# Kernel optimization log

Hardware: AMD Instinct MI355X
Metric: run time of the kernel (lower is better)

Reference implementation:

```python
import jax, jax.numpy as jnp
import numpy as np
import math

B, T, C = 64, 1024, 12
D, H, L = 512, 8, 2
FFN = 4 * D
FC_HIDDEN, NUM_CLASSES = 256, 5
KERNEL = 25          # config.moving_average default
FACTOR = 3           # config.autocorrelation_factor default
TOP_K = int(FACTOR * math.log(T))
EPS = 1e-5
MIN_SCALE = 1e-10


def _sinusoidal_pos(n_pos, dim):
    # HF AutoformerSinusoidalPositionalEmbedding._init_weight (Marian-style: sin block then cos block)
    pos = np.arange(n_pos, dtype=np.float64)[:, None]
    j = np.arange(dim)[None, :]
    enc = pos / np.power(10000.0, 2 * (j // 2) / dim)
    half = dim // 2
    out = np.zeros((n_pos, dim), np.float32)
    out[:, :half] = np.sin(enc[:, 0::2])
    out[:, half:] = np.cos(enc[:, 1::2])
    return jnp.asarray(out)


def _layernorm(x, g, b):
    mu = jnp.mean(x, axis=-1, keepdims=True)
    var = jnp.mean(jnp.square(x - mu), axis=-1, keepdims=True)
    return (x - mu) * jax.lax.rsqrt(var + EPS) * g + b


def _series_decomp_seasonal(x):
    # moving-average trend with edge-replication padding; return seasonal = x - trend
    pad = (KERNEL - 1) // 2
    xp = jnp.pad(x, ((0, 0), (pad, pad), (0, 0)), mode='edge')
    cs = jnp.cumsum(xp, axis=1)
    cs = jnp.concatenate([jnp.zeros_like(cs[:, :1]), cs], axis=1)
    trend = (cs[:, KERNEL:] - cs[:, :-KERNEL]) / KERNEL
    return x - trend


def _autocorr_attention(h, w, b):
    # w: (4, D, D) q/k/v/out, b: (4, D). Eval-mode HF AutoformerAttention (per-batch delays).
    hd = D // H
    def split(t):
        return t.reshape(B, T, H, hd).transpose(0, 2, 1, 3)  # (B,H,T,hd)
    q = split(h @ w[0] + b[0])
    k = split(h @ w[1] + b[1])
    v = split(h @ w[2] + b[2])
    # period-based dependency discovery via FFT cross-correlation along time
    qf = jnp.fft.rfft(q, n=T, axis=2)
    kf = jnp.fft.rfft(k, n=T, axis=2)
    corr = jnp.fft.irfft(qf * jnp.conj(kf), n=T, axis=2)  # (B,H,T,hd)
    mean_corr = corr.mean(axis=(1, 3))                    # (B,T)
    top_vals, top_idx = jax.lax.top_k(mean_corr, TOP_K)   # (B,K)
    wts = jax.nn.softmax(top_vals, axis=-1)               # (B,K)
    t_idx = jnp.arange(T)
    agg = jnp.zeros_like(v)
    for i in range(TOP_K):  # small fixed K, mirrors HF loop; circular roll by -delay
        idx = (t_idx[None, :] + top_idx[:, i][:, None]) % T      # (B,T)
        rolled = jnp.take_along_axis(v, idx[:, None, :, None], axis=2)
        agg = agg + rolled * wts[:, i][:, None, None, None]
    out = agg.transpose(0, 2, 1, 3).reshape(B, T, D)
    return out @ w[3] + b[3]


def _forward(x, emb_w, emb_ln_g, emb_ln_b, attn_w, attn_b, ln_g, ln_b,
             fc1_w, fc1_b, fc2_w, fc2_b, head_w1, head_b1, head_w2, head_b2):
    # AutoformerMeanScaler (observed mask is all-ones): scale = mean |x| over time, loc = 0
    scale = jnp.clip(jnp.mean(jnp.abs(x), axis=1, keepdims=True), MIN_SCALE)  # (B,1,C)
    inputs = x / scale
    # static features: log1p(|loc|)=0 and log(scale), broadcast over time; lags=[0] -> lagged == inputs
    static = jnp.concatenate([jnp.zeros_like(scale), jnp.log(scale)], axis=-1)  # (B,1,2C)
    feats = jnp.broadcast_to(static, (B, T, 2 * C))
    ti = jnp.concatenate([inputs, feats], axis=-1)  # (B,T,3C)

    h = ti @ emb_w + _sinusoidal_pos(T, D)[None]
    h = _layernorm(h, emb_ln_g, emb_ln_b)

    for l in range(L):
        res = h
        a = _autocorr_attention(h, attn_w[l], attn_b[l])
        h = _layernorm(res + a, ln_g[l, 0], ln_b[l, 0])
        h = _series_decomp_seasonal(h)
        res = h
        f = jax.nn.gelu(h @ fc1_w[l] + fc1_b[l], approximate=False)
        h = res + f @ fc2_w[l] + fc2_b[l]
        h = _layernorm(h, ln_g[l, 1], ln_b[l, 1])
        h = _series_decomp_seasonal(h)

    feat = h.mean(axis=1)  # (B,D)
    return jax.nn.relu(feat @ head_w1 + head_b1) @ head_w2 + head_b2  # (B,num_classes)


def setup_inputs() -> dict:
    key = jax.random.key(0)
    ks = jax.random.split(key, 8)
    s = 0.02
    rn = lambda k, shape: jax.random.normal(k, shape, jnp.float32) * s
    return {
        'x': jax.random.normal(ks[0], (B, T, C), jnp.float32),
        'emb_w': rn(ks[1], (3 * C, D)),
        'emb_ln_g': jnp.ones((D,), jnp.float32),
        'emb_ln_b': jnp.zeros((D,), jnp.float32),
        'attn_w': rn(ks[2], (L, 4, D, D)),
        'attn_b': jnp.zeros((L, 4, D), jnp.float32),
        'ln_g': jnp.ones((L, 2, D), jnp.float32),
        'ln_b': jnp.zeros((L, 2, D), jnp.float32),
        'fc1_w': rn(ks[3], (L, D, FFN)),
        'fc1_b': jnp.zeros((L, FFN), jnp.float32),
        'fc2_w': rn(ks[4], (L, FFN, D)),
        'fc2_b': jnp.zeros((L, D), jnp.float32),
        'head_w1': rn(ks[5], (D, FC_HIDDEN)),
        'head_b1': jnp.zeros((FC_HIDDEN,), jnp.float32),
        'head_w2': rn(ks[6], (FC_HIDDEN, NUM_CLASSES)),
        'head_b2': jnp.zeros((NUM_CLASSES,), jnp.float32),
    }


def reference(x, emb_w, emb_ln_g, emb_ln_b, attn_w, attn_b, ln_g, ln_b,
              fc1_w, fc1_b, fc2_w, fc2_b, head_w1, head_b1, head_w2, head_b2):
    return _forward(x, emb_w, emb_ln_g, emb_ln_b, attn_w, attn_b, ln_g, ln_b,
                    fc1_w, fc1_b, fc2_w, fc2_b, head_w1, head_b1, head_w2, head_b2)
```

## Files before the change

kernel.cpp:

```cpp
#include <hip/hip_runtime.h>
#include <math.h>

#define CB 64
#define CT 1024
#define CCH 12
#define CD 512
#define CL 2
#define CFFN 2048
#define CFCH 256
#define CNC 5
#define CTOPK 20
#define CEPS 1e-5f

typedef __attribute__((ext_vector_type(8))) short bfrag;
typedef __attribute__((ext_vector_type(4))) float ffrag;

__device__ inline ushort bf16r(float f) {
  unsigned u = __float_as_uint(f);
  unsigned r = (u + 0x7FFFu + ((u >> 16) & 1u)) >> 16;
  return (ushort)r;
}
__device__ inline float bf16f(ushort h) { return __uint_as_float(((unsigned)h) << 16); }

__device__ __forceinline__ void gld16(const ushort* g, ushort* l) {
  __builtin_amdgcn_global_load_lds((__attribute__((address_space(1))) void*)g,
                                   (__attribute__((address_space(3))) void*)l,
                                   16, 0, 0);
}

struct c32 { float x, y; };
__device__ inline c32 cadd(c32 a, c32 b) { return c32{a.x + b.x, a.y + b.y}; }
__device__ inline c32 csub(c32 a, c32 b) { return c32{a.x - b.x, a.y - b.y}; }
__device__ inline c32 cmul(c32 a, c32 b) {
  return c32{a.x * b.x - a.y * b.y, a.x * b.y + a.y * b.x};
}
__device__ inline c32 cmulj(c32 a, c32 b) {
  return c32{a.x * b.x + a.y * b.y, a.y * b.x - a.x * b.y};
}
__device__ inline c32 mineg_i(c32 a) { return c32{a.y, -a.x}; }
__device__ inline c32 mul_i(c32 a) { return c32{-a.y, a.x}; }

#define ZIDX(p) ((p) + ((p) >> 4))

__device__ inline int drev4(int t) {
  return ((t & 3) << 8) | (((t >> 2) & 3) << 6) | (((t >> 4) & 3) << 4) |
         (((t >> 6) & 3) << 2) | ((t >> 8) & 3);
}

template <int INV>
__device__ inline void fft_stage(c32* zz, const c32* twl, int tid, int s) {
  int L = 1 << (2 * s);
  int j = tid & (L - 1);
  int g = tid >> (2 * s);
  int p0 = (g << (2 * s + 2)) + j;
  int tb = j << (8 - 2 * s);
  c32 w1 = twl[ZIDX(tb)], w2 = twl[ZIDX(2 * tb)], w3 = twl[ZIDX(3 * tb)];
  c32 b0 = zz[ZIDX(p0)], b1 = zz[ZIDX(p0 + L)], b2 = zz[ZIDX(p0 + 2 * L)],
      b3 = zz[ZIDX(p0 + 3 * L)];
  if (INV) { b1 = cmulj(b1, w1); b2 = cmulj(b2, w2); b3 = cmulj(b3, w3); }
  else     { b1 = cmul(b1, w1);  b2 = cmul(b2, w2);  b3 = cmul(b3, w3); }
  c32 e0 = cadd(b0, b2), e1 = csub(b0, b2), e2 = cadd(b1, b3), e3 = csub(b1, b3);
  c32 e3r = INV ? mul_i(e3) : mineg_i(e3);
  zz[ZIDX(p0)] = cadd(e0, e2);
  zz[ZIDX(p0 + L)] = cadd(e1, e3r);
  zz[ZIDX(p0 + 2 * L)] = csub(e0, e2);
  zz[ZIDX(p0 + 3 * L)] = csub(e1, e3r);
}

__device__ inline void unp_acc(const c32* zf, int w, c32& acc) {
  int wc = (1024 - w) & 1023;
  c32 Z1 = zf[ZIDX(w)];
  c32 Z2r = zf[ZIDX(wc)];
  c32 Z2 = c32{Z2r.x, -Z2r.y};
  c32 Qf = c32{0.5f * (Z1.x + Z2.x), 0.5f * (Z1.y + Z2.y)};
  c32 M = c32{Z1.x - Z2.x, Z1.y - Z2.y};
  c32 Kf = c32{0.5f * M.y, -0.5f * M.x};
  acc.x += Qf.x * Kf.x + Qf.y * Kf.y;
  acc.y += Qf.y * Kf.x - Qf.x * Kf.y;
}

__global__ __launch_bounds__(256) void k_twid(c32* __restrict__ tw) {
  int j = blockIdx.x * 256 + threadIdx.x;
  double a = -2.0 * 3.14159265358979323846 * (double)j / 1024.0;
  tw[j] = c32{(float)cos(a), (float)sin(a)};
}

__global__ __launch_bounds__(256) void k_scale(const float* __restrict__ x,
                                               float* __restrict__ sc,
                                               float* __restrict__ lg) {
  int b = blockIdx.x, tid = threadIdx.x;
  float acc[CCH];
#pragma unroll
  for (int c = 0; c < CCH; ++c) acc[c] = 0.f;
  const float* xb = x + (size_t)b * CT * CCH;
  for (int t = tid; t < CT; t += 256) {
    const float* row = xb + t * CCH;
#pragma unroll
    for (int c = 0; c < CCH; ++c) acc[c] += fabsf(row[c]);
  }
  __shared__ float red[256][CCH];
#pragma unroll
  for (int c = 0; c < CCH; ++c) red[tid][c] = acc[c];
  __syncthreads();
  for (int off = 128; off > 0; off >>= 1) {
    if (tid < off) {
#pragma unroll
      for (int c = 0; c < CCH; ++c) red[tid][c] += red[tid + off][c];
    }
    __syncthreads();
  }
  if (tid < CCH) {
    float s = fmaxf(red[0][tid] * (1.0f / CT), 1e-10f);
    sc[b * CCH + tid] = s;
    lg[b * CCH + tid] = logf(s);
  }
}

__global__ __launch_bounds__(512) void k_postab(float* __restrict__ pos) {
  int t = blockIdx.x;
  int d = threadIdx.x;
  double v;
  if (d < 256) {
    double w = pow(10000.0, -((double)d) / 256.0);
    v = sin((double)t * w);
  } else {
    double w = pow(10000.0, -((double)(d - 256)) / 256.0);
    v = cos((double)t * w);
  }
  pos[(size_t)t * CD + d] = (float)v;
}

__global__ __launch_bounds__(128) void k_embed(const float* __restrict__ x,
                                               const float* __restrict__ sc,
                                               const float* __restrict__ lg,
                                               const float* __restrict__ W,
                                               const float* __restrict__ postab,
                                               const float* __restrict__ g,
                                               const float* __restrict__ beta,
                                               float* __restrict__ h,
                                               ushort* __restrict__ h2) {
  int row = blockIdx.x;
  int b = row >> 10, t = row & 1023;
  int tid = threadIdx.x;
  __shared__ float xs[CCH], ls[CCH];
  if (tid < CCH) {
    float s = sc[b * CCH + tid];
    xs[tid] = x[(size_t)row * CCH + tid] / s;
    ls[tid] = lg[b * CCH + tid];
  }
  __syncthreads();
  int d0 = tid * 4;
  float4 p = *(const float4*)(postab + (size_t)t * CD + d0);
  float v0 = p.x, v1 = p.y, v2 = p.z, v3 = p.w;
#pragma unroll
  for (int c = 0; c < CCH; ++c) {
    float xc = xs[c], lc = ls[c];
    float4 w0 = *(const float4*)(W + (size_t)c * CD + d0);
    float4 w1 = *(const float4*)(W + (size_t)(24 + c) * CD + d0);
    v0 += xc * w0.x + lc * w1.x;
    v1 += xc * w0.y + lc * w1.y;
    v2 += xc * w0.z + lc * w1.z;
    v3 += xc * w0.w + lc * w1.w;
  }
  float s1 = v0 + v1 + v2 + v3;
  float s2 = v0 * v0 + v1 * v1 + v2 * v2 + v3 * v3;
  for (int off = 32; off > 0; off >>= 1) {
    s1 += __shfl_down(s1, off);
    s2 += __shfl_down(s2, off);
  }
  __shared__ float ws1[2], ws2[2], mv[2];
  int wid = tid >> 6, lane = tid & 63;
  if (lane == 0) { ws1[wid] = s1; ws2[wid] = s2; }
  __syncthreads();
  if (tid == 0) {
    float S1 = ws1[0] + ws1[1], S2 = ws2[0] + ws2[1];
    float mu = S1 * (1.0f / CD);
    float var = S2 * (1.0f / CD) - mu * mu;
    mv[0] = mu;
    mv[1] = 1.0f / sqrtf(var + CEPS);
  }
  __syncthreads();
  float mu = mv[0], ri = mv[1];
  float4 gg = *(const float4*)(g + d0);
  float4 bb = *(const float4*)(beta + d0);
  float4 o;
  o.x = (v0 - mu) * ri * gg.x + bb.x;
  o.y = (v1 - mu) * ri * gg.y + bb.y;
  o.z = (v2 - mu) * ri * gg.z + bb.z;
  o.w = (v3 - mu) * ri * gg.w + bb.w;
  *(float4*)(h + (size_t)row * CD + d0) = o;
  ushort4 hv = {bf16r(o.x), bf16r(o.y), bf16r(o.z), bf16r(o.w)};
  *(ushort4*)(h2 + (size_t)row * CD + d0) = hv;
}

__global__ __launch_bounds__(256) void k_cvtw(const float* __restrict__ W,
                                              ushort* __restrict__ W2,
                                              int K, int N) {
  __shared__ float tile[32][33];
  int tx = threadIdx.x & 31, ty = threadIdx.x >> 5;
  int n0 = blockIdx.x * 32, k0 = blockIdx.y * 32;
#pragma unroll
  for (int r = 0; r < 4; ++r)
    tile[ty * 4 + r][tx] = W[(size_t)(k0 + ty * 4 + r) * N + n0 + tx];
  __syncthreads();
#pragma unroll
  for (int r = 0; r < 4; ++r) {
    int nl = ty * 4 + r, kl = tx;
    W2[(size_t)(n0 + nl) * K + k0 + kl] = bf16r(tile[kl][nl]);
  }
}

template <int EPI>
__global__ __launch_bounds__(256) void k_gemm3(const ushort* __restrict__ A,
                                               const ushort* __restrict__ W,
                                               const float* __restrict__ bias,
                                               const float* __restrict__ R,
                                               float* __restrict__ Cf,
                                               ushort* __restrict__ Cs,
                                               ushort* __restrict__ Cs2,
                                               int lda, int ldb, int ldc, int K) {
  __shared__ ushort AhS[2][128 * 32];
  __shared__ ushort BhS[2][128 * 32];
  int tid = threadIdx.x;
  int nx = gridDim.x;
  int nwg = nx * gridDim.y;
  int flat = blockIdx.y * nx + blockIdx.x;
  int sw = (flat & 7) * (nwg >> 3) + (flat >> 3);
  int n0 = (sw % nx) * 128, m0 = (sw / nx) * 128;
  int wid = __builtin_amdgcn_readfirstlane(tid >> 6);
  int lane = tid & 63;
  int lr = lane >> 2;
  int lc = ((lane & 3) ^ ((lr >> 2) & 3)) * 8;
  int wm = wid >> 1, wn = wid & 1;
  int mOff = wm * 64, nOff = wn * 64;
  int quad = lane >> 4, l16 = lane & 15;

  const ushort* pA = A + (size_t)(m0 + wid * 32 + lr) * lda + lc;
  const ushort* pB = W + (size_t)(n0 + wid * 32 + lr) * ldb + lc;
  const int NK = K >> 5;

  ffrag acc[4][4];
#pragma unroll
  for (int i = 0; i < 4; ++i)
#pragma unroll
    for (int j = 0; j < 4; ++j) acc[i][j] = (ffrag)(0.f);

#define ISSUE(t, buf)                                                        \
  {                                                                          \
    int kk = (t) << 5;                                                       \
    ushort* lA = &AhS[buf][(wid * 32) * 32];                                 \
    ushort* lB = &BhS[buf][(wid * 32) * 32];                                 \
    gld16(pA + kk, lA);                                                      \
    gld16(pA + (size_t)16 * lda + kk, lA + 16 * 32);                         \
    gld16(pB + kk, lB);                                                      \
    gld16(pB + (size_t)16 * ldb + kk, lB + 16 * 32);                         \
  }

  ISSUE(0, 0);
  ISSUE(1, 1);
  for (int k = 0; k < NK; ++k) {
    if (k + 1 < NK) {
      asm volatile("s_waitcnt vmcnt(4)\n\ts_barrier" ::: "memory");
    } else {
      asm volatile("s_waitcnt vmcnt(0)\n\ts_barrier" ::: "memory");
    }
    int buf = k & 1;
    bfrag ah[4], bh[4];
#pragma unroll
    for (int i = 0; i < 4; ++i) {
      int row = mOff + i * 16 + l16;
      ah[i] = *(const bfrag*)&AhS[buf][row * 32 + (quad ^ ((row >> 2) & 3)) * 8];
    }
#pragma unroll
    for (int j = 0; j < 4; ++j) {
      int row = nOff + j * 16 + l16;
      bh[j] = *(const bfrag*)&BhS[buf][row * 32 + (quad ^ ((row >> 2) & 3)) * 8];
    }
#pragma unroll
    for (int i = 0; i < 4; ++i)
#pragma unroll
      for (int j = 0; j < 4; ++j)
        acc[i][j] = __builtin_amdgcn_mfma_f32_16x16x32_bf16(ah[i], bh[j], acc[i][j], 0, 0, 0);
    asm volatile("s_barrier" ::: "memory");
    if (k + 2 < NK) ISSUE(k + 2, buf);
  }
#undef ISSUE

#pragma unroll
  for (int j = 0; j < 4; ++j) {
    int col = n0 + nOff + j * 16 + l16;
    float bcol = bias[col];
#pragma unroll
    for (int i = 0; i < 4; ++i) {
      int rowb = m0 + mOff + i * 16 + quad * 4;
      if (EPI == 7) {
        if (col < 1024) {
          float4 o = {acc[i][j][0] + bcol, acc[i][j][1] + bcol,
                      acc[i][j][2] + bcol, acc[i][j][3] + bcol};
          *(float4*)(Cf + (size_t)col * ldc + rowb) = o;
        } else {
#pragma unroll
          for (int r = 0; r < 4; ++r)
            Cs[(size_t)(rowb + r) * 512 + (col - 1024)] = bf16r(acc[i][j][r] + bcol);
        }
      } else {
#pragma unroll
        for (int r = 0; r < 4; ++r) {
          int row = rowb + r;
          float vv = acc[i][j][r] + bcol;
          if (EPI == 1) vv = 0.5f * vv * (1.0f + erff(vv * 0.7071067811865475f));
          if (EPI == 2) vv += R[(size_t)row * ldc + col];
          if (EPI == 1) {
            Cs[(size_t)row * ldc + col] = bf16r(vv);
          } else {
            Cf[(size_t)row * ldc + col] = vv;
          }
        }
      }
    }
  }
}

__global__ __launch_bounds__(256) void k_fft(const float* __restrict__ QT,
                                             const c32* __restrict__ twg,
                                             c32* __restrict__ part, int Mc) {
  __shared__ c32 z[4][1088];
  __shared__ c32 twl[1088];
  int dg = blockIdx.x, zb = blockIdx.y, tid = threadIdx.x;
#pragma unroll
  for (int k = 0; k < 4; ++k) {
    int i = tid + k * 256;
    twl[ZIDX(i)] = twg[i];
  }
  c32 pa = {0.f, 0.f}, pb = {0.f, 0.f}, p5 = {0.f, 0.f};
  for (int i = 0; i < 4; ++i) {
    int d0 = dg * 16 + i * 4;
#pragma unroll
    for (int f = 0; f < 4; ++f) {
      const float* qr = QT + (size_t)(d0 + f) * Mc + (size_t)zb * 1024;
      const float* kr = QT + (size_t)(512 + d0 + f) * Mc + (size_t)zb * 1024;
#pragma unroll
      for (int k = 0; k < 4; ++k) {
        int t = tid + k * 256;
        z[f][ZIDX(drev4(t))] = c32{qr[t], kr[t]};
      }
    }
    __syncthreads();
    for (int s = 0; s < 5; ++s) {
#pragma unroll
      for (int f = 0; f < 4; ++f) fft_stage<0>(&z[f][0], twl, tid, s);
      __syncthreads();
    }
#pragma unroll
    for (int f = 0; f < 4; ++f) {
      unp_acc(&z[f][0], tid, pa);
      unp_acc(&z[f][0], tid + 256, pb);
      if (tid == 0) unp_acc(&z[f][0], 512, p5);
    }
    __syncthreads();
  }
  c32* po = part + ((size_t)zb * 32 + dg) * 513;
  po[tid] = pa;
  po[tid + 256] = pb;
  if (tid == 0) po[512] = p5;
}

__global__ __launch_bounds__(256) void k_spectopk(const c32* __restrict__ part,
                                                  const c32* __restrict__ twg,
                                                  float* __restrict__ wts,
                                                  int* __restrict__ idxs) {
  int b = blockIdx.x, tid = threadIdx.x;
  __shared__ c32 twl[1088];
  __shared__ c32 S[1024];
  __shared__ c32 zz[1088];
  __shared__ float corr[1024];
#pragma unroll
  for (int k = 0; k < 4; ++k) {
    int i = tid + k * 256;
    twl[ZIDX(i)] = twg[i];
  }
  c32 sa = {0.f, 0.f}, sb = {0.f, 0.f}, s5 = {0.f, 0.f};
  const c32* pbase = part + (size_t)b * 32 * 513;
  for (int p = 0; p < 32; ++p) {
    const c32* pp = pbase + p * 513;
    sa = cadd(sa, pp[tid]);
    sb = cadd(sb, pp[tid + 256]);
    if (tid == 0) s5 = cadd(s5, pp[512]);
  }
  S[tid] = sa;
  S[tid + 256] = sb;
  if (tid == 0) S[512] = s5;
  if (tid > 0) S[1024 - tid] = c32{sa.x, -sa.y};
  S[768 - tid] = c32{sb.x, -sb.y};
  __syncthreads();
#pragma unroll
  for (int k = 0; k < 4; ++k) {
    int t = tid + k * 256;
    zz[ZIDX(drev4(t))] = S[t];
  }
  __syncthreads();
  for (int s = 0; s < 5; ++s) {
    fft_stage<1>(&zz[0], twl, tid, s);
    __syncthreads();
  }
  const float scl = 1.0f / (1024.0f * 512.0f);
#pragma unroll
  for (int k = 0; k < 4; ++k) {
    int t = tid + k * 256;
    corr[t] = zz[ZIDX(t)].x * scl;
  }
  __syncthreads();
  __shared__ float swv[4];
  __shared__ int swi[4];
  __shared__ float selv[CTOPK];
  __shared__ int seli[CTOPK];
  int wid = tid >> 6, lane = tid & 63;
  for (int k = 0; k < CTOPK; ++k) {
    float bv = -INFINITY;
    int bi = 0;
#pragma unroll
    for (int q = 0; q < 4; ++q) {
      int idx = tid + q * 256;
      float v = corr[idx];
      if (v > bv || (v == bv && idx < bi)) { bv = v; bi = idx; }
    }
#pragma unroll
    for (int off = 32; off > 0; off >>= 1) {
      float ov = __shfl_down(bv, off);
      int oi = __shfl_down(bi, off);
      if (ov > bv || (ov == bv && oi < bi)) { bv = ov; bi = oi; }
    }
    if (lane == 0) { swv[wid] = bv; swi[wid] = bi; }
    __syncthreads();
    if (tid == 0) {
      float mvv = swv[0];
      int mi = swi[0];
      for (int q2 = 1; q2 < 4; ++q2)
        if (swv[q2] > mvv || (swv[q2] == mvv && swi[q2] < mi)) { mvv = swv[q2]; mi = swi[q2]; }
      selv[k] = mvv;
      seli[k] = mi;
      corr[mi] = -INFINITY;
    }
    __syncthreads();
  }
  if (tid == 0) {
    float mx = selv[0], sum = 0.f, e[CTOPK];
    for (int k = 0; k < CTOPK; ++k) {
      e[k] = expf(selv[k] - mx);
      sum += e[k];
    }
    float inv = 1.0f / sum;
    for (int k = 0; k < CTOPK; ++k) {
      wts[b * CTOPK + k] = e[k] * inv;
      idxs[b * CTOPK + k] = seli[k];
    }
  }
}

__global__ __launch_bounds__(128) void k_agg(const ushort* __restrict__ Vf,
                                             const float* __restrict__ wts,
                                             const int* __restrict__ idxs,
                                             ushort* __restrict__ out2) {
  int nb = gridDim.x;
  int blk = blockIdx.x;
  int row = (blk & 7) * (nb >> 3) + (blk >> 3);
  int b = row >> 10, t = row & 1023;
  int d0 = threadIdx.x * 4;
  const ushort* Vb = Vf + (size_t)b * CT * 512;
  float4 acc = {0.f, 0.f, 0.f, 0.f};
#pragma unroll
  for (int k = 0; k < CTOPK; ++k) {
    float w = wts[b * CTOPK + k];
    int r = t + idxs[b * CTOPK + k];
    if (r >= CT) r -= CT;
    ushort4 v = *(const ushort4*)(Vb + (size_t)r * 512 + d0);
    acc.x += w * bf16f(v.x);
    acc.y += w * bf16f(v.y);
    acc.z += w * bf16f(v.z);
    acc.w += w * bf16f(v.w);
  }
  ushort4 hv = {bf16r(acc.x), bf16r(acc.y), bf16r(acc.z), bf16r(acc.w)};
  *(ushort4*)(out2 + (size_t)row * CD + d0) = hv;
}

__global__ __launch_bounds__(128) void k_stats(const float* __restrict__ X,
                                               c32* __restrict__ st) {
  int row = blockIdx.x, tid = threadIdx.x;
  int d0 = tid * 4;
  float4 v = *(const float4*)(X + (size_t)row * CD + d0);
  float s1 = v.x + v.y + v.z + v.w;
  float s2 = v.x * v.x + v.y * v.y + v.z * v.z + v.w * v.w;
  for (int off = 32; off > 0; off >>= 1) {
    s1 += __shfl_down(s1, off);
    s2 += __shfl_down(s2, off);
  }
  __shared__ float ws1[2], ws2[2];
  int wid = tid >> 6, lane = tid & 63;
  if (lane == 0) { ws1[wid] = s1; ws2[wid] = s2; }
  __syncthreads();
  if (tid == 0) {
    float S1 = ws1[0] + ws1[1], S2 = ws2[0] + ws2[1];
    float mu = S1 * (1.0f / CD);
    float var = S2 * (1.0f / CD) - mu * mu;
    st[row] = c32{mu, 1.0f / sqrtf(var + CEPS)};
  }
}

__global__ __launch_bounds__(256) void k_dec2(const float* __restrict__ X,
                                              const c32* __restrict__ st,
                                              const float* __restrict__ g,
                                              float* __restrict__ out,
                                              ushort* __restrict__ out2) {
  int b = blockIdx.y;
  int t0 = blockIdx.x * 64;
  int tid = threadIdx.x;
  const float* xb = X + (size_t)b * CT * CD;
  const c32* sb = st + (size_t)b * CT;
  float g0v = g[tid], g1v = g[tid + 256];
  float s0 = 0.f, s1 = 0.f;
#pragma unroll
  for (int j = -12; j <= 12; ++j) {
    int u = t0 + j;
    u = u < 0 ? 0 : (u > CT - 1 ? CT - 1 : u);
    c32 ms = sb[u];
    s0 += (xb[(size_t)u * CD + tid] - ms.x) * ms.y;
    s1 += (xb[(size_t)u * CD + tid + 256] - ms.x) * ms.y;
  }
  const float inv = 1.0f / 25.0f;
  for (int tt = 0; tt < 64; ++tt) {
    int t = t0 + tt;
    c32 mc = sb[t];
    float z0 = (xb[(size_t)t * CD + tid] - mc.x) * mc.y;
    float z1 = (xb[(size_t)t * CD + tid + 256] - mc.x) * mc.y;
    float o0 = g0v * (z0 - s0 * inv);
    float o1 = g1v * (z1 - s1 * inv);
    size_t ro = (size_t)(b * CT + t) * CD;
    out[ro + tid] = o0;
    out[ro + tid + 256] = o1;
    out2[ro + tid] = bf16r(o0);
    out2[ro + tid + 256] = bf16r(o1);
    int ua = t + 13;
    ua = ua > CT - 1 ? CT - 1 : ua;
    int ur = t - 12;
    ur = ur < 0 ? 0 : ur;
    c32 ma = sb[ua], mr = sb[ur];
    s0 += (xb[(size_t)ua * CD + tid] - ma.x) * ma.y -
          (xb[(size_t)ur * CD + tid] - mr.x) * mr.y;
    s1 += (xb[(size_t)ua * CD + tid + 256] - ma.x) * ma.y -
          (xb[(size_t)ur * CD + tid + 256] - mr.x) * mr.y;
  }
}

__global__ __launch_bounds__(256) void k_meanp(const float* __restrict__ X,
                                               float* __restrict__ part) {
  int b = blockIdx.x, g = blockIdx.y, tid = threadIdx.x;
  const float* xb = X + (size_t)b * CT * CD + (size_t)g * 128 * CD;
  float a0 = 0.f, a1 = 0.f;
  for (int r = 0; r < 128; ++r) {
    a0 += xb[(size_t)r * CD + tid];
    a1 += xb[(size_t)r * CD + tid + 256];
  }
  part[((size_t)b * 8 + g) * CD + tid] = a0;
  part[((size_t)b * 8 + g) * CD + tid + 256] = a1;
}

__global__ __launch_bounds__(256) void k_headf(const float* __restrict__ part,
                                               const float* __restrict__ w1,
                                               const float* __restrict__ b1,
                                               const float* __restrict__ w2,
                                               const float* __restrict__ b2,
                                               float* __restrict__ out) {
  int b = blockIdx.x, tid = threadIdx.x;
  __shared__ float f[CD];
  __shared__ float hid[CFCH];
  for (int d = tid; d < CD; d += 256) {
    float s = 0.f;
#pragma unroll
    for (int g = 0; g < 8; ++g) s += part[((size_t)b * 8 + g) * CD + d];
    f[d] = s * (1.0f / CT);
  }
  __syncthreads();
  float a = b1[tid];
  for (int d = 0; d < CD; ++d) a += f[d] * w1[d * CFCH + tid];
  hid[tid] = fmaxf(a, 0.f);
  __syncthreads();
  if (tid < CNC) {
    float a2 = b2[tid];
    for (int j = 0; j < CFCH; ++j) a2 += hid[j] * w2[j * CNC + tid];
    out[b * CNC + tid] = a2;
  }
}

extern "C" void kernel_launch(void* const* d_in, const int* in_sizes, int n_in,
                              void* d_out, int out_size, void* d_ws, size_t ws_size,
                              hipStream_t stream) {
  const float* x = (const float*)d_in[0];
  const float* emb_w = (const float*)d_in[1];
  const float* emb_g = (const float*)d_in[2];
  const float* emb_b = (const float*)d_in[3];
  const float* attn_w = (const float*)d_in[4];
  const float* attn_b = (const float*)d_in[5];
  const float* ln_g = (const float*)d_in[6];
  const float* ln_bb = (const float*)d_in[7];
  const float* fc1_w = (const float*)d_in[8];
  const float* fc1_b = (const float*)d_in[9];
  const float* fc2_w = (const float*)d_in[10];
  const float* fc2_b = (const float*)d_in[11];
  const float* hw1 = (const float*)d_in[12];
  const float* hb1 = (const float*)d_in[13];
  const float* hw2 = (const float*)d_in[14];
  const float* hb2 = (const float*)d_in[15];
  float* outp = (float*)d_out;

  const size_t WQ = 262144ULL;
  const size_t LW = 4 * WQ + 1048576ULL + 1048576ULL;
  const size_t W2TOT = CL * LW;

  const size_t FIXED_B = W2TOT * 2
                         + (size_t)CT * CD * 4
                         + 2 * (size_t)CB * CCH * 4
                         + 2 * (size_t)CB * CTOPK * 4
                         + (size_t)CB * 8 * CD * 4
                         + 1024 * 8
                         + 4096;
  const size_t PERB = 2ULL * CT * CD * 4 + (size_t)CT * CD * 2 + (size_t)CT * 2048 * 2 +
                      (size_t)32 * 513 * 8 + (size_t)CT * 8;
  int Bc = CB;
  while (Bc > 1) {
    if ((size_t)Bc * PERB + FIXED_B <= ws_size) break;
    Bc >>= 1;
  }
  const size_t CHF = (size_t)Bc * CT * CD;

  char* wsp = (char*)d_ws;
  float* P0 = (float*)wsp;     wsp += CHF * 4;
  float* P1 = (float*)wsp;     wsp += CHF * 4;
  ushort* U0 = (ushort*)wsp;   wsp += CHF * 2;
  ushort* U1 = (ushort*)wsp;   wsp += (size_t)Bc * CT * 2048 * 2;
  ushort* W2b = (ushort*)wsp;  wsp += W2TOT * 2;
  float* postab = (float*)wsp; wsp += (size_t)CT * CD * 4;
  float* scb = (float*)wsp;    wsp += (size_t)CB * CCH * 4;
  float* lgb = (float*)wsp;    wsp += (size_t)CB * CCH * 4;
  float* wtb = (float*)wsp;    wsp += (size_t)CB * CTOPK * 4;
  int* idb = (int*)wsp;        wsp += (size_t)CB * CTOPK * 4;
  float* partb = (float*)wsp;  wsp += (size_t)CB * 8 * CD * 4;
  c32* twc = (c32*)wsp;        wsp += 1024 * sizeof(c32);
  c32* partc = (c32*)wsp;      wsp += (size_t)Bc * 32 * 513 * sizeof(c32);
  c32* stb = (c32*)wsp;        wsp += (size_t)Bc * CT * sizeof(c32);

  for (int l = 0; l < CL; ++l) {
    ushort* wq2 = W2b + l * LW;
    ushort* wo2 = wq2 + 3 * WQ;
    ushort* w12 = wo2 + WQ;
    ushort* w22 = w12 + 1048576;
    for (int m = 0; m < 4; ++m)
      k_cvtw<<<dim3(CD / 32, CD / 32), 256, 0, stream>>>(
          attn_w + ((size_t)(l * 4 + m)) * CD * CD, wq2 + m * WQ, CD, CD);
    k_cvtw<<<dim3(CFFN / 32, CD / 32), 256, 0, stream>>>(
        fc1_w + (size_t)l * CD * CFFN, w12, CD, CFFN);
    k_cvtw<<<dim3(CD / 32, CFFN / 32), 256, 0, stream>>>(
        fc2_w + (size_t)l * CFFN * CD, w22, CFFN, CD);
  }

  k_scale<<<CB, 256, 0, stream>>>(x, scb, lgb);
  k_postab<<<CT, 512, 0, stream>>>(postab);
  k_twid<<<4, 256, 0, stream>>>(twc);

  for (int b0 = 0; b0 < CB; b0 += Bc) {
    const int Mc = Bc * CT;

    float* HP = P0;
    float* SA = P1;

    k_embed<<<Mc, 128, 0, stream>>>(x + (size_t)b0 * CT * CCH, scb + b0 * CCH,
                                    lgb + b0 * CCH, emb_w, postab, emb_g, emb_b,
                                    HP, U0);

    for (int l = 0; l < CL; ++l) {
      const float* bqkv = attn_b + (size_t)l * 4 * CD;
      const float* bo = attn_b + (size_t)(l * 4 + 3) * CD;
      const float* g0 = ln_g + (size_t)(l * 2 + 0) * CD;
      const float* g1 = ln_g + (size_t)(l * 2 + 1) * CD;
      const float* B1 = fc1_b + (size_t)l * CFFN;
      const float* B2f = fc2_b + (size_t)l * CD;
      const ushort* wq2 = W2b + l * LW;
      const ushort* wo2 = wq2 + 3 * WQ;
      const ushort* w12 = wo2 + WQ;
      const ushort* w22 = w12 + 1048576;

      k_gemm3<7><<<dim3(1536 / 128, Mc / 128), 256, 0, stream>>>(
          U0, wq2, bqkv, nullptr, (float*)U1, (ushort*)SA, nullptr, CD, CD, Mc, CD);
      k_fft<<<dim3(32, Bc), 256, 0, stream>>>((const float*)U1, twc, partc, Mc);
      k_spectopk<<<Bc, 256, 0, stream>>>(partc, twc, wtb, idb);
      k_agg<<<Mc, 128, 0, stream>>>((const ushort*)SA, wtb, idb, U0);
      k_gemm3<2><<<dim3(CD / 128, Mc / 128), 256, 0, stream>>>(
          U0, wo2, bo, HP, (float*)SA, nullptr, nullptr, CD, CD, CD, CD);
      k_stats<<<Mc, 128, 0, stream>>>((float*)SA, stb);
      k_dec2<<<dim3(CT / 64, Bc), 256, 0, stream>>>((float*)SA, stb, g0, HP, U0);
      k_gemm3<1><<<dim3(CFFN / 128, Mc / 128), 256, 0, stream>>>(
          U0, w12, B1, nullptr, nullptr, U1, nullptr, CD, CD, CFFN, CD);
      k_gemm3<2><<<dim3(CD / 128, Mc / 128), 256, 0, stream>>>(
          U1, w22, B2f, HP, (float*)SA, nullptr, nullptr, CFFN, CFFN, CD, CFFN);
      k_stats<<<Mc, 128, 0, stream>>>((float*)SA, stb);
      k_dec2<<<dim3(CT / 64, Bc), 256, 0, stream>>>((float*)SA, stb, g1, HP, U0);
    }

    k_meanp<<<dim3(Bc, 8), 256, 0, stream>>>(HP, partb + (size_t)b0 * 8 * CD);
    k_headf<<<Bc, 256, 0, stream>>>(partb + (size_t)b0 * 8 * CD, hw1, hb1, hw2, hb2,
                                    outp + (size_t)b0 * CNC);
  }
}
```

Measured before the change: 2.848 ms.

## Fuse residual-add row statistics into GEMM epilogue and batch weight conversion

The out-projection and FC2 GEMM epilogues now compute per-row partial sum and sum-of-squares alongside the residual add. The partials are reduced across lanes and written to an 8-slot buffer, and a small finalize kernel turns them into mean and inverse std. This replaces the separate k_stats pass that re-read the full fp32 activations. The change also merges the four attention weight conversions into one launch via a z grid dimension and adds a launch-bounds occupancy hint to the GEMM, which may raise register pressure.

```diff
diff --git a/kernel.cpp b/kernel.cpp
--- a/kernel.cpp
+++ b/kernel.cpp
@@ -197,28 +197,29 @@
                                               ushort* __restrict__ W2,
                                               int K, int N) {
   __shared__ float tile[32][33];
+  size_t zoff = (size_t)blockIdx.z * K * N;
   int tx = threadIdx.x & 31, ty = threadIdx.x >> 5;
   int n0 = blockIdx.x * 32, k0 = blockIdx.y * 32;
 #pragma unroll
   for (int r = 0; r < 4; ++r)
-    tile[ty * 4 + r][tx] = W[(size_t)(k0 + ty * 4 + r) * N + n0 + tx];
+    tile[ty * 4 + r][tx] = W[zoff + (size_t)(k0 + ty * 4 + r) * N + n0 + tx];
   __syncthreads();
 #pragma unroll
   for (int r = 0; r < 4; ++r) {
     int nl = ty * 4 + r, kl = tx;
-    W2[(size_t)(n0 + nl) * K + k0 + kl] = bf16r(tile[kl][nl]);
+    W2[zoff + (size_t)(n0 + nl) * K + k0 + kl] = bf16r(tile[kl][nl]);
   }
 }
 
 template <int EPI>
-__global__ __launch_bounds__(256) void k_gemm3(const ushort* __restrict__ A,
-                                               const ushort* __restrict__ W,
-                                               const float* __restrict__ bias,
-                                               const float* __restrict__ R,
-                                               float* __restrict__ Cf,
-                                               ushort* __restrict__ Cs,
-                                               ushort* __restrict__ Cs2,
-                                               int lda, int ldb, int ldc, int K) {
+__global__ __launch_bounds__(256, 4) void k_gemm3(const ushort* __restrict__ A,
+                                                  const ushort* __restrict__ W,
+                                                  const float* __restrict__ bias,
+                                                  const float* __restrict__ R,
+                                                  float* __restrict__ Cf,
+                                                  ushort* __restrict__ Cs,
+                                                  ushort* __restrict__ Cs2,
+                                                  int lda, int ldb, int ldc, int K) {
   __shared__ ushort AhS[2][128 * 32];
   __shared__ ushort BhS[2][128 * 32];
   int tid = threadIdx.x;
@@ -286,39 +287,80 @@
   }
 #undef ISSUE
 
-#pragma unroll
-  for (int j = 0; j < 4; ++j) {
-    int col = n0 + nOff + j * 16 + l16;
-    float bcol = bias[col];
+  if (EPI == 3) {
+    c32* st8 = (c32*)Cs2;
 #pragma unroll
     for (int i = 0; i < 4; ++i) {
-      int rowb = m0 + mOff + i * 16 + quad * 4;
-      if (EPI == 7) {
-        if (col < 1024) {
-          float4 o = {acc[i][j][0] + bcol, acc[i][j][1] + bcol,
-                      acc[i][j][2] + bcol, acc[i][j][3] + bcol};
-          *(float4*)(Cf + (size_t)col * ldc + rowb) = o;
+#pragma unroll
+      for (int r = 0; r < 4; ++r) {
+        int row = m0 + mOff + i * 16 + quad * 4 + r;
+        float s1 = 0.f, s2 = 0.f;
+#pragma unroll
+        for (int j = 0; j < 4; ++j) {
+          int col = n0 + nOff + j * 16 + l16;
+          float vv = acc[i][j][r] + bias[col] + R[(size_t)row * ldc + col];
+          Cf[(size_t)row * ldc + col] = vv;
+          s1 += vv;
+          s2 += vv * vv;
+        }
+#pragma unroll
+        for (int off = 8; off > 0; off >>= 1) {
+          s1 += __shfl_xor(s1, off);
+          s2 += __shfl_xor(s2, off);
+        }
+        if (l16 == 0) st8[(size_t)row * 8 + (n0 >> 6) + wn] = c32{s1, s2};
+      }
+    }
+  } else {
+#pragma unroll
+    for (int j = 0; j < 4; ++j) {
+      int col = n0 + nOff + j * 16 + l16;
+      float bcol = bias[col];
+#pragma unroll
+      for (int i = 0; i < 4; ++i) {
+        int rowb = m0 + mOff + i * 16 + quad * 4;
+        if (EPI == 7) {
+          if (col < 1024) {
+            float4 o = {acc[i][j][0] + bcol, acc[i][j][1] + bcol,
+                        acc[i][j][2] + bcol, acc[i][j][3] + bcol};
+            *(float4*)(Cf + (size_t)col * ldc + rowb) = o;
+          } else {
+#pragma unroll
+            for (int r = 0; r < 4; ++r)
+              Cs[(size_t)(rowb + r) * 512 + (col - 1024)] = bf16r(acc[i][j][r] + bcol);
+          }
         } else {
 #pragma unroll
-          for (int r = 0; r < 4; ++r)
-            Cs[(size_t)(rowb + r) * 512 + (col - 1024)] = bf16r(acc[i][j][r] + bcol);
-        }
-      } else {
-#pragma unroll
-        for (int r = 0; r < 4; ++r) {
-          int row = rowb + r;
-          float vv = acc[i][j][r] + bcol;
-          if (EPI == 1) vv = 0.5f * vv * (1.0f + erff(vv * 0.7071067811865475f));
-          if (EPI == 2) vv += R[(size_t)row * ldc + col];
-          if (EPI == 1) {
-            Cs[(size_t)row * ldc + col] = bf16r(vv);
-          } else {
-            Cf[(size_t)row * ldc + col] = vv;
+          for (int r = 0; r < 4; ++r) {
+            int row = rowb + r;
+            float vv = acc[i][j][r] + bcol;
+            if (EPI == 1) vv = 0.5f * vv * (1.0f + erff(vv * 0.7071067811865475f));
+            if (EPI == 2) vv += R[(size_t)row * ldc + col];
+            if (EPI == 1) {
+              Cs[(size_t)row * ldc + col] = bf16r(vv);
+            } else {
+              Cf[(size_t)row * ldc + col] = vv;
+            }
           }
         }
       }
     }
   }
+}
+
+__global__ __launch_bounds__(256) void k_finst(const c32* __restrict__ st8,
+                                               c32* __restrict__ st) {
+  int row = blockIdx.x * 256 + threadIdx.x;
+  float s1 = 0.f, s2 = 0.f;
+#pragma unroll
+  for (int p = 0; p < 8; ++p) {
+    c32 v = st8[(size_t)row * 8 + p];
+    s1 += v.x;
+    s2 += v.y;
+  }
+  float mu = s1 * (1.0f / CD);
+  float var = s2 * (1.0f / CD) - mu * mu;
+  st[row] = c32{mu, 1.0f / sqrtf(var + CEPS)};
 }
 
 __global__ __launch_bounds__(256) void k_fft(const float* __restrict__ QT,
@@ -481,29 +523,6 @@
   }
   ushort4 hv = {bf16r(acc.x), bf16r(acc.y), bf16r(acc.z), bf16r(acc.w)};
   *(ushort4*)(out2 + (size_t)row * CD + d0) = hv;
-}
-
-__global__ __launch_bounds__(128) void k_stats(const float* __restrict__ X,
-                                               c32* __restrict__ st) {
-  int row = blockIdx.x, tid = threadIdx.x;
-  int d0 = tid * 4;
-  float4 v = *(const float4*)(X + (size_t)row * CD + d0);
-  float s1 = v.x + v.y + v.z + v.w;
-  float s2 = v.x * v.x + v.y * v.y + v.z * v.z + v.w * v.w;
-  for (int off = 32; off > 0; off >>= 1) {
-    s1 += __shfl_down(s1, off);
-    s2 += __shfl_down(s2, off);
-  }
-  __shared__ float ws1[2], ws2[2];
-  int wid = tid >> 6, lane = tid & 63;
-  if (lane == 0) { ws1[wid] = s1; ws2[wid] = s2; }
-  __syncthreads();
-  if (tid == 0) {
-    float S1 = ws1[0] + ws1[1], S2 = ws2[0] + ws2[1];
-    float mu = S1 * (1.0f / CD);
-    float var = S2 * (1.0f / CD) - mu * mu;
-    st[row] = c32{mu, 1.0f / sqrtf(var + CEPS)};
-  }
 }
 
 __global__ __launch_bounds__(256) void k_dec2(const float* __restrict__ X,
@@ -624,7 +643,7 @@
                          + 1024 * 8
                          + 4096;
   const size_t PERB = 2ULL * CT * CD * 4 + (size_t)CT * CD * 2 + (size_t)CT * 2048 * 2 +
-                      (size_t)32 * 513 * 8 + (size_t)CT * 8;
+                      (size_t)32 * 513 * 8 + (size_t)CT * 8 + (size_t)CT * 64;
   int Bc = CB;
   while (Bc > 1) {
     if ((size_t)Bc * PERB + FIXED_B <= ws_size) break;
@@ -647,18 +666,17 @@
   c32* twc = (c32*)wsp;        wsp += 1024 * sizeof(c32);
   c32* partc = (c32*)wsp;      wsp += (size_t)Bc * 32 * 513 * sizeof(c32);
   c32* stb = (c32*)wsp;        wsp += (size_t)Bc * CT * sizeof(c32);
+  c32* st8b = (c32*)wsp;       wsp += (size_t)Bc * CT * 8 * sizeof(c32);
 
   for (int l = 0; l < CL; ++l) {
     ushort* wq2 = W2b + l * LW;
-    ushort* wo2 = wq2 + 3 * WQ;
-    ushort* w12 = wo2 + WQ;
+    ushort* w12 = wq2 + 4 * WQ;
     ushort* w22 = w12 + 1048576;
-    for (int m = 0; m < 4; ++m)
-      k_cvtw<<<dim3(CD / 32, CD / 32), 256, 0, stream>>>(
-          attn_w + ((size_t)(l * 4 + m)) * CD * CD, wq2 + m * WQ, CD, CD);
-    k_cvtw<<<dim3(CFFN / 32, CD / 32), 256, 0, stream>>>(
+    k_cvtw<<<dim3(CD / 32, CD / 32, 4), 256, 0, stream>>>(
+        attn_w + (size_t)l * 4 * CD * CD, wq2, CD, CD);
+    k_cvtw<<<dim3(CFFN / 32, CD / 32, 1), 256, 0, stream>>>(
         fc1_w + (size_t)l * CD * CFFN, w12, CD, CFFN);
-    k_cvtw<<<dim3(CD / 32, CFFN / 32), 256, 0, stream>>>(
+    k_cvtw<<<dim3(CD / 32, CFFN / 32, 1), 256, 0, stream>>>(
         fc2_w + (size_t)l * CFFN * CD, w22, CFFN, CD);
   }
 
@@ -685,7 +703,7 @@
       const float* B2f = fc2_b + (size_t)l * CD;
       const ushort* wq2 = W2b + l * LW;
       const ushort* wo2 = wq2 + 3 * WQ;
-      const ushort* w12 = wo2 + WQ;
+      const ushort* w12 = wq2 + 4 * WQ;
       const ushort* w22 = w12 + 1048576;
 
       k_gemm3<7><<<dim3(1536 / 128, Mc / 128), 256, 0, stream>>>(
@@ -693,15 +711,15 @@
       k_fft<<<dim3(32, Bc), 256, 0, stream>>>((const float*)U1, twc, partc, Mc);
       k_spectopk<<<Bc, 256, 0, stream>>>(partc, twc, wtb, idb);
       k_agg<<<Mc, 128, 0, stream>>>((const ushort*)SA, wtb, idb, U0);
-      k_gemm3<2><<<dim3(CD / 128, Mc / 128), 256, 0, stream>>>(
-          U0, wo2, bo, HP, (float*)SA, nullptr, nullptr, CD, CD, CD, CD);
-      k_stats<<<Mc, 128, 0, stream>>>((float*)SA, stb);
+      k_gemm3<3><<<dim3(CD / 128, Mc / 128), 256, 0, stream>>>(
+          U0, wo2, bo, HP, (float*)SA, nullptr, (ushort*)st8b, CD, CD, CD, CD);
+      k_finst<<<Mc / 256, 256, 0, stream>>>(st8b, stb);
       k_dec2<<<dim3(CT / 64, Bc), 256, 0, stream>>>((float*)SA, stb, g0, HP, U0);
       k_gemm3<1><<<dim3(CFFN / 128, Mc / 128), 256, 0, stream>>>(
           U0, w12, B1, nullptr, nullptr, U1, nullptr, CD, CD, CFFN, CD);
-      k_gemm3<2><<<dim3(CD / 128, Mc / 128), 256, 0, stream>>>(
-          U1, w22, B2f, HP, (float*)SA, nullptr, nullptr, CFFN, CFFN, CD, CFFN);
-      k_stats<<<Mc, 128, 0, stream>>>((float*)SA, stb);
+      k_gemm3<3><<<dim3(CD / 128, Mc / 128), 256, 0, stream>>>(
+          U1, w22, B2f, HP, (float*)SA, nullptr, (ushort*)st8b, CFFN, CFFN, CD, CFFN);
+      k_finst<<<Mc / 256, 256, 0, stream>>>(st8b, stb);
       k_dec2<<<dim3(CT / 64, Bc), 256, 0, stream>>>((float*)SA, stb, g1, HP, U0);
     }
 
```

Result: no change. 2.864 ms (+0.6%).
